# Optimization experiments

Hardware: AMD Instinct MI355X
Metric: run time of the kernel (lower is better)

The kernel has to match this reference:

```python
import jax, jax.numpy as jnp
import numpy as np

ANCHORS = np.array([[10,13],[16,30],[33,23],[30,61],[62,45],[59,119],[116,90],[156,198],[373,326]], dtype=np.float32)
ANCHOR_MASK = [[6,7,8],[3,4,5],[0,1,2]]
N_CLASSES = 80
IGNORE_THRESH = 0.5
MAX_TRUE = 128  # padded per-image GT box budget (replaces dynamic boolean indexing)


def _bce(logits, targets):
    # BCEWithLogits, elementwise: softplus(x) - x*z
    return jax.nn.softplus(logits) - logits * targets


def _decode(fm, anchors, input_shape):
    # fm: [B, A*(5+C), H, W] -> grid, raw [B,H,W,A,5+C], pred_xy, pred_wh
    B, _, H, W = fm.shape
    A = anchors.shape[0]
    raw = fm.reshape(B, A, 5 + N_CLASSES, H, W).transpose(0, 3, 4, 1, 2)
    gy, gx = jnp.meshgrid(jnp.arange(H, dtype=fm.dtype), jnp.arange(W, dtype=fm.dtype), indexing='ij')
    grid = jnp.stack([gx, gy], axis=-1)[None, :, :, None, :]  # [1,H,W,1,2] (x,y)
    gs = jnp.array([H, W], dtype=fm.dtype)
    pred_xy = (jax.nn.sigmoid(raw[..., :2]) + grid) / gs
    pred_wh = anchors[None, None, None, :, :] * jnp.exp(raw[..., 2:4]) / input_shape
    return grid, raw, pred_xy, pred_wh


def _gather_true(yt):
    # Pad/select up to MAX_TRUE GT boxes per image (object_mask == 1 cells).
    B = yt.shape[0]
    boxes = yt[..., :4].reshape(B, -1, 4)
    mask = yt[..., 4].reshape(B, -1)
    idx = jnp.argsort(-mask, axis=1)[:, :MAX_TRUE]            # positives first
    tb = jnp.take_along_axis(boxes, idx[..., None], axis=1)   # [B,K,4]
    valid = jnp.take_along_axis(mask, idx, axis=1) == 1.0     # [B,K]
    return tb, valid


def _best_iou(pred_box, tb, valid):
    # pred_box [B,H,W,A,4] (xywh), tb [B,K,4] -> best IoU over valid GT [B,H,W,A]
    p = pred_box[:, :, :, :, None, :]
    t = tb[:, None, None, None, :, :]
    p_min, p_max = p[..., :2] - p[..., 2:4] / 2, p[..., :2] + p[..., 2:4] / 2
    t_min, t_max = t[..., :2] - t[..., 2:4] / 2, t[..., :2] + t[..., 2:4] / 2
    inter = jnp.clip(jnp.minimum(p_max, t_max) - jnp.maximum(p_min, t_min), 0.0)
    inter_a = inter[..., 0] * inter[..., 1]
    pa = p[..., 2] * p[..., 3]
    ta = t[..., 2] * t[..., 3]
    iou = inter_a / (pa + ta - inter_a)
    iou = jnp.where(valid[:, None, None, None, :], iou, 0.0)
    return jnp.max(iou, axis=-1)


def _scale_loss(fm, yt, s, input_shape):
    B = fm.shape[0]
    anchors = jnp.asarray(ANCHORS[ANCHOR_MASK[s]])
    grid, raw, pxy, pwh = _decode(fm, anchors, input_shape)
    pred_box = jnp.concatenate([pxy, pwh], axis=-1)
    obj = yt[..., 4:5]
    tcls = yt[..., 5:]
    H, W = fm.shape[2], fm.shape[3]
    gs = jnp.array([H, W], dtype=fm.dtype)
    raw_txy = yt[..., :2] * gs - grid
    ratio = yt[..., 2:4] / anchors[None, None, None, :, :] * input_shape
    raw_twh = jnp.where(obj == 0, 0.0, jnp.log(jnp.where(obj == 0, 1.0, ratio)))
    box_scale = 2.0 - yt[..., 2:3] * yt[..., 3:4]
    tb, valid = _gather_true(yt)
    ignore = (_best_iou(pred_box, tb, valid) < IGNORE_THRESH).astype(fm.dtype)[..., None]
    xy_l = jnp.sum(obj * box_scale * _bce(raw[..., 0:2], raw_txy)) / B
    wh_l = jnp.sum(obj * box_scale * (raw[..., 2:4] - raw_twh) ** 2) / B
    bc = _bce(raw[..., 4:5], obj)
    conf_l = jnp.sum(obj * bc + (1.0 - obj) * bc * ignore) / B
    cls_l = jnp.sum(obj * _bce(raw[..., 5:], tcls)) / B
    return xy_l, wh_l, conf_l, cls_l


def _make_y_true(k, B, S):
    k1, k2, k3, k4 = jax.random.split(k, 4)
    xy = jax.random.uniform(k1, (B, S, S, 3, 2), minval=0.02, maxval=0.98)
    wh = jax.random.uniform(k2, (B, S, S, 3, 2), minval=0.02, maxval=0.4)
    obj = (jax.random.uniform(k3, (B, S, S, 3, 1)) < 0.005).astype(jnp.float32)
    cls = jax.nn.one_hot(jax.random.randint(k4, (B, S, S, 3), 0, N_CLASSES), N_CLASSES)
    return jnp.concatenate([xy, wh, obj, cls * obj], axis=-1)


def setup_inputs() -> dict:
    key = jax.random.key(0)
    ks = jax.random.split(key, 6)
    B = 16
    return {
        'yolo_out_0': jax.random.normal(ks[0], (B, 255, 19, 19), jnp.float32),
        'yolo_out_1': jax.random.normal(ks[1], (B, 255, 38, 38), jnp.float32),
        'yolo_out_2': jax.random.normal(ks[2], (B, 255, 76, 76), jnp.float32),
        'y_true_0': _make_y_true(ks[3], B, 19),
        'y_true_1': _make_y_true(ks[4], B, 38),
        'y_true_2': _make_y_true(ks[5], B, 76),
    }


def reference(yolo_out_0, yolo_out_1, yolo_out_2, y_true_0, y_true_1, y_true_2):
    outs = [yolo_out_0, yolo_out_1, yolo_out_2]
    yts = [y_true_0, y_true_1, y_true_2]
    input_shape = jnp.array([outs[0].shape[2] * 32, outs[0].shape[3] * 32], dtype=outs[0].dtype)
    lxy = lwh = lconf = lcls = 0.0
    for s in range(3):
        a, b, c, d = _scale_loss(outs[s], yts[s], s, input_shape)
        lxy, lwh, lconf, lcls = lxy + a, lwh + b, lconf + c, lcls + d
    total = lxy + lwh + lconf + lcls
    # [total, xy, wh, conf, class] (each was unsqueeze(0)'d in torch)
    return jnp.stack([total, lxy, lwh, lconf, lcls])
```

## Files before the change

### kernel.cpp

```cpp
#include <hip/hip_runtime.h>

#define MAX_TRUE 128

__device__ const float d_anch[3][3][2] = {
    {{116.f, 90.f}, {156.f, 198.f}, {373.f, 326.f}},
    {{30.f, 61.f}, {62.f, 45.f}, {59.f, 119.f}},
    {{10.f, 13.f}, {16.f, 30.f}, {33.f, 23.f}},
};

__device__ __forceinline__ float softplusf_(float x) {
    return fmaxf(x, 0.0f) + log1pf(expf(-fabsf(x)));
}
__device__ __forceinline__ float bcef_(float l, float t) {
    return softplusf_(l) - l * t;
}
__device__ __forceinline__ float sigmoidf_(float x) {
    return 1.0f / (1.0f + expf(-x));
}

__global__ void cand_kernel(const float* __restrict__ yt0, const float* __restrict__ yt1,
                            const float* __restrict__ yt2,
                            unsigned char* __restrict__ objmask,
                            float* __restrict__ chunkdata, int* __restrict__ chunkcnt) {
    __shared__ int wcnt[4];
    int bid = blockIdx.x, tid = threadIdx.x;
    int wid = tid >> 6, lane = tid & 63;
    int b, chunk, spb, objofs;
    const float* yt;
    if (bid < 80)       { b = bid / 5;  chunk = bid - b * 5;  spb = 1083;  objofs = 0;     yt = yt0; }
    else if (bid < 352) { int l = bid - 80;  b = l / 17; chunk = l - b * 17; spb = 4332;  objofs = 17328; yt = yt1; }
    else                { int l = bid - 352; b = l / 68; chunk = l - b * 68; spb = 17328; objofs = 86640; yt = yt2; }
    int cell = chunk * 256 + tid;
    bool valid = cell < spb;
    const float* src = yt + ((size_t)b * spb + cell) * 85;
    float obj = valid ? src[4] : 0.f;
    bool isobj = obj > 0.5f;
    if (valid) objmask[objofs + b * spb + cell] = isobj ? 1 : 0;
    unsigned long long m = __ballot(isobj);
    int wofs = __popcll(m & ((1ull << lane) - 1ull));
    if (lane == 0) wcnt[wid] = __popcll(m);
    __syncthreads();
    int base = 0;
    #pragma unroll
    for (int i = 0; i < 4; ++i) if (i < wid) base += wcnt[i];
    if (isobj) {
        int pos = base + wofs;
        float* d = chunkdata + ((size_t)bid * 256 + pos) * 5;
        d[0] = src[0];
        d[1] = src[1];
        d[2] = src[2];
        d[3] = src[3];
        ((int*)d)[4] = cell;
    }
    if (tid == 0) chunkcnt[bid] = wcnt[0] + wcnt[1] + wcnt[2] + wcnt[3];
}

__global__ void fused_kernel(const float* __restrict__ fm0, const float* __restrict__ fm1,
                             const float* __restrict__ fm2,
                             const float* __restrict__ yt0, const float* __restrict__ yt1,
                             const float* __restrict__ yt2,
                             const unsigned char* __restrict__ objmask,
                             const float* __restrict__ chunkdata, const int* __restrict__ chunkcnt,
                             float* __restrict__ partials, float* __restrict__ objpart) {
    __shared__ float4 sA[MAX_TRUE];
    __shared__ float sT[MAX_TRUE];
    __shared__ float wred[4][4];
    __shared__ int cnts[68];
    __shared__ int pre[69];
    int bid = blockIdx.x, tid = threadIdx.x;
    int wid = tid >> 6, lane = tid & 63;

    if (bid < 1488) {
        int s, local, lnb, Sdim, objofs, spb;
        const float* fm;
        if (bid < 96)       { s = 0; local = bid;       lnb = 2;  Sdim = 19; objofs = 0;     spb = 1083;  fm = fm0; }
        else if (bid < 384) { s = 1; local = bid - 96;  lnb = 6;  Sdim = 38; objofs = 17328; spb = 4332;  fm = fm1; }
        else                { s = 2; local = bid - 384; lnb = 23; Sdim = 76; objofs = 86640; spb = 17328; fm = fm2; }
        int ba = local / lnb;
        int chunk = local - ba * lnb;
        int a = ba % 3, b = ba / 3;
        int cbase, nch;
        if (s == 0)      { cbase = b * 5;        nch = 5;  }
        else if (s == 1) { cbase = 80 + b * 17;  nch = 17; }
        else             { cbase = 352 + b * 68; nch = 68; }
        if (tid < nch) cnts[tid] = chunkcnt[cbase + tid];
        __syncthreads();
        if (tid == 0) {
            int acc = 0;
            for (int c = 0; c < nch; ++c) { pre[c] = acc; acc += cnts[c]; }
            pre[nch] = acc;
        }
        __syncthreads();
        int total = pre[nch];
        int t128 = min(total, MAX_TRUE);
        if (tid < nch) {
            int n = cnts[tid], p0 = pre[tid];
            for (int j = 0; j < n; ++j) {
                int p = p0 + j;
                if (p >= MAX_TRUE) break;
                const float* e = chunkdata + ((size_t)(cbase + tid) * 256 + j) * 5;
                float x = e[0], y = e[1], w = e[2], h = e[3];
                float4 r;
                r.x = x - 0.5f * w; r.y = y - 0.5f * h;
                r.z = x + 0.5f * w; r.w = y + 0.5f * h;
                sA[p] = r;
                sT[p] = w * h;
            }
        }
        for (int p = t128 + tid; p < MAX_TRUE; p += 256) {
            sA[p] = make_float4(0.f, 0.f, 0.f, 0.f);
            sT[p] = 0.f;
        }
        __syncthreads();
        int kr = (t128 + 3) & ~3;
        int HW = Sdim * Sdim;
        int hw = chunk * 256 + tid;
        float lconf = 0.f;
        if (hw < HW) {
            int ob = objmask[objofs + b * spb + hw * 3 + a];
            const float* f = fm + ((size_t)(b * 255 + a * 85)) * HW + hw;
            float l0 = f[0], l1 = f[(size_t)HW], l2 = f[2 * (size_t)HW],
                  l3 = f[3 * (size_t)HW], l4 = f[4 * (size_t)HW];
            if (!ob) {
                int h = hw / Sdim, w = hw - h * Sdim;
                float aw = d_anch[s][a][0], ah = d_anch[s][a][1];
                const float inv_in = 1.0f / 608.0f;
                float px = (sigmoidf_(l0) + (float)w) / (float)Sdim;
                float py = (sigmoidf_(l1) + (float)h) / (float)Sdim;
                float pw = aw * expf(l2) * inv_in;
                float ph = ah * expf(l3) * inv_in;
                float pminx = px - 0.5f * pw, pmaxx = px + 0.5f * pw;
                float pminy = py - 0.5f * ph, pmaxy = py + 0.5f * ph;
                float pa = pw * ph;
                float m0 = 0.f, m1 = 0.f, m2 = 0.f, m3 = 0.f;
                for (int i = 0; i < kr; i += 4) {
                    float4 b0 = sA[i], b1 = sA[i + 1], b2 = sA[i + 2], b3 = sA[i + 3];
                    float t0 = sT[i], t1 = sT[i + 1], t2 = sT[i + 2], t3 = sT[i + 3];
                    float ix, iy;
                    ix = fmaxf(fminf(pmaxx, b0.z) - fmaxf(pminx, b0.x), 0.f);
                    iy = fmaxf(fminf(pmaxy, b0.w) - fmaxf(pminy, b0.y), 0.f);
                    m0 = fmaxf(m0, fmaf(3.0f, ix * iy, -t0));
                    ix = fmaxf(fminf(pmaxx, b1.z) - fmaxf(pminx, b1.x), 0.f);
                    iy = fmaxf(fminf(pmaxy, b1.w) - fmaxf(pminy, b1.y), 0.f);
                    m1 = fmaxf(m1, fmaf(3.0f, ix * iy, -t1));
                    ix = fmaxf(fminf(pmaxx, b2.z) - fmaxf(pminx, b2.x), 0.f);
                    iy = fmaxf(fminf(pmaxy, b2.w) - fmaxf(pminy, b2.y), 0.f);
                    m2 = fmaxf(m2, fmaf(3.0f, ix * iy, -t2));
                    ix = fmaxf(fminf(pmaxx, b3.z) - fmaxf(pminx, b3.x), 0.f);
                    iy = fmaxf(fminf(pmaxy, b3.w) - fmaxf(pminy, b3.y), 0.f);
                    m3 = fmaxf(m3, fmaf(3.0f, ix * iy, -t3));
                }
                float m = fmaxf(fmaxf(m0, m1), fmaxf(m2, m3));
                lconf = (m < pa) ? softplusf_(l4) : 0.f;
            }
        }
        #pragma unroll
        for (int o = 32; o > 0; o >>= 1)
            lconf += __shfl_down(lconf, o);
        if (lane == 0) wred[wid][0] = lconf;
        __syncthreads();
        if (tid == 0)
            partials[bid] = wred[0][0] + wred[1][0] + wred[2][0] + wred[3][0];
    } else {
        int cid = bid - 1488;
        int n = chunkcnt[cid];
        float* op = objpart + (size_t)cid * 4;
        if (n == 0) {
            if (tid == 0) { op[0] = 0.f; op[1] = 0.f; op[2] = 0.f; op[3] = 0.f; }
            return;
        }
        int s, b, spb, Sdim;
        const float *fm, *yt;
        if (cid < 80)       { s = 0; b = cid / 5;  spb = 1083;  Sdim = 19; fm = fm0; yt = yt0; }
        else if (cid < 352) { int l = cid - 80;  s = 1; b = l / 17; spb = 4332;  Sdim = 38; fm = fm1; yt = yt1; }
        else                { int l = cid - 352; s = 2; b = l / 68; spb = 17328; Sdim = 76; fm = fm2; yt = yt2; }
        int HW = Sdim * Sdim;
        float axy = 0.f, awh = 0.f, aconf = 0.f, acls = 0.f;
        for (int ci = wid; ci < n; ci += 4) {
            const float* cd = chunkdata + ((size_t)cid * 256 + ci) * 5;
            float x = cd[0], y = cd[1], w = cd[2], h = cd[3];
            int cell = ((const int*)cd)[4];
            int hw = cell / 3, a = cell - hw * 3;
            int hh = hw / Sdim, ww = hw - hh * Sdim;
            const float* f = fm + ((size_t)(b * 255 + a * 85)) * HW + hw;
            const float* yrow = yt + ((size_t)b * spb + cell) * 85;
            float cl = bcef_(f[(size_t)(5 + lane) * HW], yrow[5 + lane]);
            if (lane < 16) {
                int k2 = 64 + lane;
                cl += bcef_(f[(size_t)(5 + k2) * HW], yrow[5 + k2]);
            }
            acls += cl;
            float bscale = 2.f - w * h;
            if (lane < 5) {
                float lv = f[(size_t)lane * HW];
                if (lane == 0) axy += bscale * bcef_(lv, x * (float)Sdim - (float)ww);
                else if (lane == 1) axy += bscale * bcef_(lv, y * (float)Sdim - (float)hh);
                else if (lane == 2) {
                    float tw = logf(w / d_anch[s][a][0] * 608.f);
                    float d = lv - tw;
                    awh += bscale * d * d;
                } else if (lane == 3) {
                    float th = logf(h / d_anch[s][a][1] * 608.f);
                    float d = lv - th;
                    awh += bscale * d * d;
                } else {
                    aconf += bcef_(lv, 1.0f);
                }
            }
        }
        #pragma unroll
        for (int o = 32; o > 0; o >>= 1) {
            axy += __shfl_down(axy, o);
            awh += __shfl_down(awh, o);
            aconf += __shfl_down(aconf, o);
            acls += __shfl_down(acls, o);
        }
        if (lane == 0) {
            wred[wid][0] = axy; wred[wid][1] = awh;
            wred[wid][2] = aconf; wred[wid][3] = acls;
        }
        __syncthreads();
        if (tid == 0) {
            op[0] = wred[0][0] + wred[1][0] + wred[2][0] + wred[3][0];
            op[1] = wred[0][1] + wred[1][1] + wred[2][1] + wred[3][1];
            op[2] = wred[0][2] + wred[1][2] + wred[2][2] + wred[3][2];
            op[3] = wred[0][3] + wred[1][3] + wred[2][3] + wred[3][3];
        }
    }
}

__global__ void finalize_kernel(const float* __restrict__ partials,
                                const float* __restrict__ objpart,
                                float* __restrict__ out) {
    __shared__ float red[4][5];
    int tid = threadIdx.x;
    int wid = tid >> 6, lane = tid & 63;
    float cno = 0.f;
    for (int i = tid; i < 1488; i += 256) cno += partials[i];
    float xy = 0.f, wh = 0.f, co = 0.f, cl = 0.f;
    for (int i = tid; i < 1440; i += 256) {
        const float* op = objpart + (size_t)i * 4;
        xy += op[0]; wh += op[1]; co += op[2]; cl += op[3];
    }
    #pragma unroll
    for (int o = 32; o > 0; o >>= 1) {
        cno += __shfl_down(cno, o);
        xy += __shfl_down(xy, o);
        wh += __shfl_down(wh, o);
        co += __shfl_down(co, o);
        cl += __shfl_down(cl, o);
    }
    if (lane == 0) {
        red[wid][0] = cno; red[wid][1] = xy; red[wid][2] = wh;
        red[wid][3] = co;  red[wid][4] = cl;
    }
    __syncthreads();
    if (tid == 0) {
        float conf = 0.f, txy = 0.f, twh = 0.f, tcl = 0.f;
        for (int i = 0; i < 4; ++i) {
            conf += red[i][0] + red[i][3];
            txy += red[i][1]; twh += red[i][2]; tcl += red[i][4];
        }
        const float invB = 1.0f / 16.0f;
        float a0 = txy * invB;
        float a1 = twh * invB;
        float a2 = conf * invB;
        float a3 = tcl * invB;
        out[1] = a0; out[2] = a1; out[3] = a2; out[4] = a3;
        out[0] = a0 + a1 + a2 + a3;
    }
}

extern "C" void kernel_launch(void* const* d_in, const int* in_sizes, int n_in,
                              void* d_out, int out_size, void* d_ws, size_t ws_size,
                              hipStream_t stream) {
    const float* fm0 = (const float*)d_in[0];
    const float* fm1 = (const float*)d_in[1];
    const float* fm2 = (const float*)d_in[2];
    const float* yt0 = (const float*)d_in[3];
    const float* yt1 = (const float*)d_in[4];
    const float* yt2 = (const float*)d_in[5];
    float* out = (float*)d_out;

    char* ws = (char*)d_ws;
    int* chunkcnt = (int*)ws;
    float* partials = (float*)(ws + 5760);
    float* objpart = (float*)(ws + 11712);
    unsigned char* objmask = (unsigned char*)(ws + 34752);
    float* chunkdata = (float*)(ws + 398656);

    cand_kernel<<<1440, 256, 0, stream>>>(yt0, yt1, yt2, objmask, chunkdata, chunkcnt);
    fused_kernel<<<2928, 256, 0, stream>>>(fm0, fm1, fm2, yt0, yt1, yt2,
                                           objmask, chunkdata, chunkcnt, partials, objpart);
    finalize_kernel<<<1, 256, 0, stream>>>(partials, objpart, out);
}
```

Baseline: 41.32 us.

## Fuse object-cell loss computation into candidate compaction kernel

Moves the per-positive-cell xy/wh/conf/class loss work out of the second kernel and into the candidate-compaction kernel, reading the compacted boxes from shared memory instead of re-reading them from global memory. The second kernel now handles only the no-object confidence/IoU blocks, so its grid shrinks from 2928 to 1488 blocks. This shortens the second launch at the cost of a heavier first kernel that now also reads feature maps and uses extra shared memory.

```diff
diff --git a/kernel.cpp b/kernel.cpp
--- a/kernel.cpp
+++ b/kernel.cpp
@@ -18,18 +18,25 @@
     return 1.0f / (1.0f + expf(-x));
 }
 
-__global__ void cand_kernel(const float* __restrict__ yt0, const float* __restrict__ yt1,
-                            const float* __restrict__ yt2,
-                            unsigned char* __restrict__ objmask,
-                            float* __restrict__ chunkdata, int* __restrict__ chunkcnt) {
+__global__ void cand_obj_kernel(const float* __restrict__ yt0, const float* __restrict__ yt1,
+                                const float* __restrict__ yt2,
+                                const float* __restrict__ fm0, const float* __restrict__ fm1,
+                                const float* __restrict__ fm2,
+                                unsigned char* __restrict__ objmask,
+                                float* __restrict__ chunkdata, int* __restrict__ chunkcnt,
+                                float* __restrict__ objpart) {
     __shared__ int wcnt[4];
+    __shared__ float sc[256][5];
+    __shared__ float wred[4][4];
     int bid = blockIdx.x, tid = threadIdx.x;
     int wid = tid >> 6, lane = tid & 63;
-    int b, chunk, spb, objofs;
-    const float* yt;
-    if (bid < 80)       { b = bid / 5;  chunk = bid - b * 5;  spb = 1083;  objofs = 0;     yt = yt0; }
-    else if (bid < 352) { int l = bid - 80;  b = l / 17; chunk = l - b * 17; spb = 4332;  objofs = 17328; yt = yt1; }
-    else                { int l = bid - 352; b = l / 68; chunk = l - b * 68; spb = 17328; objofs = 86640; yt = yt2; }
+    int s, b, chunk, spb, objofs;
+    const float *yt, *fm;
+    if (bid < 80)       { s = 0; b = bid / 5;  chunk = bid - b * 5;  spb = 1083;  objofs = 0;     yt = yt0; fm = fm0; }
+    else if (bid < 352) { int l = bid - 80;  s = 1; b = l / 17; chunk = l - b * 17; spb = 4332;  objofs = 17328; yt = yt1; fm = fm1; }
+    else                { int l = bid - 352; s = 2; b = l / 68; chunk = l - b * 68; spb = 17328; objofs = 86640; yt = yt2; fm = fm2; }
+    int Sdim = (s == 0) ? 19 : ((s == 1) ? 38 : 76);
+    int HW = Sdim * Sdim;
     int cell = chunk * 256 + tid;
     bool valid = cell < spb;
     const float* src = yt + ((size_t)b * spb + cell) * 85;
@@ -43,190 +50,174 @@
     int base = 0;
     #pragma unroll
     for (int i = 0; i < 4; ++i) if (i < wid) base += wcnt[i];
+    int total = wcnt[0] + wcnt[1] + wcnt[2] + wcnt[3];
     if (isobj) {
         int pos = base + wofs;
+        float x = src[0], y = src[1], w = src[2], h = src[3];
         float* d = chunkdata + ((size_t)bid * 256 + pos) * 5;
-        d[0] = src[0];
-        d[1] = src[1];
-        d[2] = src[2];
-        d[3] = src[3];
+        d[0] = x; d[1] = y; d[2] = w; d[3] = h;
         ((int*)d)[4] = cell;
-    }
-    if (tid == 0) chunkcnt[bid] = wcnt[0] + wcnt[1] + wcnt[2] + wcnt[3];
-}
-
-__global__ void fused_kernel(const float* __restrict__ fm0, const float* __restrict__ fm1,
-                             const float* __restrict__ fm2,
-                             const float* __restrict__ yt0, const float* __restrict__ yt1,
-                             const float* __restrict__ yt2,
-                             const unsigned char* __restrict__ objmask,
-                             const float* __restrict__ chunkdata, const int* __restrict__ chunkcnt,
-                             float* __restrict__ partials, float* __restrict__ objpart) {
+        sc[pos][0] = x; sc[pos][1] = y; sc[pos][2] = w; sc[pos][3] = h;
+        ((int*)sc[pos])[4] = cell;
+    }
+    if (tid == 0) chunkcnt[bid] = total;
+    __syncthreads();
+
+    float axy = 0.f, awh = 0.f, aconf = 0.f, acls = 0.f;
+    for (int ci = wid; ci < total; ci += 4) {
+        float x = sc[ci][0], y = sc[ci][1], w = sc[ci][2], h = sc[ci][3];
+        int ccell = ((int*)sc[ci])[4];
+        int hw = ccell / 3, a = ccell - hw * 3;
+        int hh = hw / Sdim, ww = hw - hh * Sdim;
+        const float* f = fm + ((size_t)(b * 255 + a * 85)) * HW + hw;
+        const float* yrow = yt + ((size_t)b * spb + ccell) * 85;
+        float cl = bcef_(f[(size_t)(5 + lane) * HW], yrow[5 + lane]);
+        if (lane < 16) {
+            int k2 = 64 + lane;
+            cl += bcef_(f[(size_t)(5 + k2) * HW], yrow[5 + k2]);
+        }
+        acls += cl;
+        float bscale = 2.f - w * h;
+        if (lane < 5) {
+            float lv = f[(size_t)lane * HW];
+            if (lane == 0) axy += bscale * bcef_(lv, x * (float)Sdim - (float)ww);
+            else if (lane == 1) axy += bscale * bcef_(lv, y * (float)Sdim - (float)hh);
+            else if (lane == 2) {
+                float tw = logf(w / d_anch[s][a][0] * 608.f);
+                float d = lv - tw;
+                awh += bscale * d * d;
+            } else if (lane == 3) {
+                float th = logf(h / d_anch[s][a][1] * 608.f);
+                float d = lv - th;
+                awh += bscale * d * d;
+            } else {
+                aconf += bcef_(lv, 1.0f);
+            }
+        }
+    }
+    #pragma unroll
+    for (int o = 32; o > 0; o >>= 1) {
+        axy += __shfl_down(axy, o);
+        awh += __shfl_down(awh, o);
+        aconf += __shfl_down(aconf, o);
+        acls += __shfl_down(acls, o);
+    }
+    if (lane == 0) {
+        wred[wid][0] = axy; wred[wid][1] = awh;
+        wred[wid][2] = aconf; wred[wid][3] = acls;
+    }
+    __syncthreads();
+    if (tid == 0) {
+        float* op = objpart + (size_t)bid * 4;
+        op[0] = wred[0][0] + wred[1][0] + wred[2][0] + wred[3][0];
+        op[1] = wred[0][1] + wred[1][1] + wred[2][1] + wred[3][1];
+        op[2] = wred[0][2] + wred[1][2] + wred[2][2] + wred[3][2];
+        op[3] = wred[0][3] + wred[1][3] + wred[2][3] + wred[3][3];
+    }
+}
+
+__global__ void conf_kernel(const float* __restrict__ fm0, const float* __restrict__ fm1,
+                            const float* __restrict__ fm2,
+                            const unsigned char* __restrict__ objmask,
+                            const float* __restrict__ chunkdata, const int* __restrict__ chunkcnt,
+                            float* __restrict__ partials) {
     __shared__ float4 sA[MAX_TRUE];
     __shared__ float sT[MAX_TRUE];
-    __shared__ float wred[4][4];
+    __shared__ float wred[4];
     __shared__ int cnts[68];
     __shared__ int pre[69];
     int bid = blockIdx.x, tid = threadIdx.x;
     int wid = tid >> 6, lane = tid & 63;
-
-    if (bid < 1488) {
-        int s, local, lnb, Sdim, objofs, spb;
-        const float* fm;
-        if (bid < 96)       { s = 0; local = bid;       lnb = 2;  Sdim = 19; objofs = 0;     spb = 1083;  fm = fm0; }
-        else if (bid < 384) { s = 1; local = bid - 96;  lnb = 6;  Sdim = 38; objofs = 17328; spb = 4332;  fm = fm1; }
-        else                { s = 2; local = bid - 384; lnb = 23; Sdim = 76; objofs = 86640; spb = 17328; fm = fm2; }
-        int ba = local / lnb;
-        int chunk = local - ba * lnb;
-        int a = ba % 3, b = ba / 3;
-        int cbase, nch;
-        if (s == 0)      { cbase = b * 5;        nch = 5;  }
-        else if (s == 1) { cbase = 80 + b * 17;  nch = 17; }
-        else             { cbase = 352 + b * 68; nch = 68; }
-        if (tid < nch) cnts[tid] = chunkcnt[cbase + tid];
-        __syncthreads();
-        if (tid == 0) {
-            int acc = 0;
-            for (int c = 0; c < nch; ++c) { pre[c] = acc; acc += cnts[c]; }
-            pre[nch] = acc;
-        }
-        __syncthreads();
-        int total = pre[nch];
-        int t128 = min(total, MAX_TRUE);
-        if (tid < nch) {
-            int n = cnts[tid], p0 = pre[tid];
-            for (int j = 0; j < n; ++j) {
-                int p = p0 + j;
-                if (p >= MAX_TRUE) break;
-                const float* e = chunkdata + ((size_t)(cbase + tid) * 256 + j) * 5;
-                float x = e[0], y = e[1], w = e[2], h = e[3];
-                float4 r;
-                r.x = x - 0.5f * w; r.y = y - 0.5f * h;
-                r.z = x + 0.5f * w; r.w = y + 0.5f * h;
-                sA[p] = r;
-                sT[p] = w * h;
+    int s, local, lnb, Sdim, objofs, spb;
+    const float* fm;
+    if (bid < 96)       { s = 0; local = bid;       lnb = 2;  Sdim = 19; objofs = 0;     spb = 1083;  fm = fm0; }
+    else if (bid < 384) { s = 1; local = bid - 96;  lnb = 6;  Sdim = 38; objofs = 17328; spb = 4332;  fm = fm1; }
+    else                { s = 2; local = bid - 384; lnb = 23; Sdim = 76; objofs = 86640; spb = 17328; fm = fm2; }
+    int ba = local / lnb;
+    int chunk = local - ba * lnb;
+    int a = ba % 3, b = ba / 3;
+    int cbase, nch;
+    if (s == 0)      { cbase = b * 5;        nch = 5;  }
+    else if (s == 1) { cbase = 80 + b * 17;  nch = 17; }
+    else             { cbase = 352 + b * 68; nch = 68; }
+    if (tid < nch) cnts[tid] = chunkcnt[cbase + tid];
+    __syncthreads();
+    if (tid == 0) {
+        int acc = 0;
+        for (int c = 0; c < nch; ++c) { pre[c] = acc; acc += cnts[c]; }
+        pre[nch] = acc;
+    }
+    __syncthreads();
+    int total = pre[nch];
+    int t128 = min(total, MAX_TRUE);
+    if (tid < nch) {
+        int n = cnts[tid], p0 = pre[tid];
+        for (int j = 0; j < n; ++j) {
+            int p = p0 + j;
+            if (p >= MAX_TRUE) break;
+            const float* e = chunkdata + ((size_t)(cbase + tid) * 256 + j) * 5;
+            float x = e[0], y = e[1], w = e[2], h = e[3];
+            float4 r;
+            r.x = x - 0.5f * w; r.y = y - 0.5f * h;
+            r.z = x + 0.5f * w; r.w = y + 0.5f * h;
+            sA[p] = r;
+            sT[p] = w * h;
+        }
+    }
+    for (int p = t128 + tid; p < MAX_TRUE; p += 256) {
+        sA[p] = make_float4(0.f, 0.f, 0.f, 0.f);
+        sT[p] = 0.f;
+    }
+    __syncthreads();
+    int kr = (t128 + 3) & ~3;
+    int HW = Sdim * Sdim;
+    int hw = chunk * 256 + tid;
+    float lconf = 0.f;
+    if (hw < HW) {
+        int ob = objmask[objofs + b * spb + hw * 3 + a];
+        const float* f = fm + ((size_t)(b * 255 + a * 85)) * HW + hw;
+        float l0 = f[0], l1 = f[(size_t)HW], l2 = f[2 * (size_t)HW],
+              l3 = f[3 * (size_t)HW], l4 = f[4 * (size_t)HW];
+        if (!ob) {
+            int h = hw / Sdim, w = hw - h * Sdim;
+            float aw = d_anch[s][a][0], ah = d_anch[s][a][1];
+            const float inv_in = 1.0f / 608.0f;
+            float px = (sigmoidf_(l0) + (float)w) / (float)Sdim;
+            float py = (sigmoidf_(l1) + (float)h) / (float)Sdim;
+            float pw = aw * expf(l2) * inv_in;
+            float ph = ah * expf(l3) * inv_in;
+            float pminx = px - 0.5f * pw, pmaxx = px + 0.5f * pw;
+            float pminy = py - 0.5f * ph, pmaxy = py + 0.5f * ph;
+            float pa = pw * ph;
+            float m0 = 0.f, m1 = 0.f, m2 = 0.f, m3 = 0.f;
+            for (int i = 0; i < kr; i += 4) {
+                float4 b0 = sA[i], b1 = sA[i + 1], b2 = sA[i + 2], b3 = sA[i + 3];
+                float t0 = sT[i], t1 = sT[i + 1], t2 = sT[i + 2], t3 = sT[i + 3];
+                float ix, iy;
+                ix = fmaxf(fminf(pmaxx, b0.z) - fmaxf(pminx, b0.x), 0.f);
+                iy = fmaxf(fminf(pmaxy, b0.w) - fmaxf(pminy, b0.y), 0.f);
+                m0 = fmaxf(m0, fmaf(3.0f, ix * iy, -t0));
+                ix = fmaxf(fminf(pmaxx, b1.z) - fmaxf(pminx, b1.x), 0.f);
+                iy = fmaxf(fminf(pmaxy, b1.w) - fmaxf(pminy, b1.y), 0.f);
+                m1 = fmaxf(m1, fmaf(3.0f, ix * iy, -t1));
+                ix = fmaxf(fminf(pmaxx, b2.z) - fmaxf(pminx, b2.x), 0.f);
+                iy = fmaxf(fminf(pmaxy, b2.w) - fmaxf(pminy, b2.y), 0.f);
+                m2 = fmaxf(m2, fmaf(3.0f, ix * iy, -t2));
+                ix = fmaxf(fminf(pmaxx, b3.z) - fmaxf(pminx, b3.x), 0.f);
+                iy = fmaxf(fminf(pmaxy, b3.w) - fmaxf(pminy, b3.y), 0.f);
+                m3 = fmaxf(m3, fmaf(3.0f, ix * iy, -t3));
             }
-        }
-        for (int p = t128 + tid; p < MAX_TRUE; p += 256) {
-            sA[p] = make_float4(0.f, 0.f, 0.f, 0.f);
-            sT[p] = 0.f;
-        }
-        __syncthreads();
-        int kr = (t128 + 3) & ~3;
-        int HW = Sdim * Sdim;
-        int hw = chunk * 256 + tid;
-        float lconf = 0.f;
-        if (hw < HW) {
-            int ob = objmask[objofs + b * spb + hw * 3 + a];
-            const float* f = fm + ((size_t)(b * 255 + a * 85)) * HW + hw;
-            float l0 = f[0], l1 = f[(size_t)HW], l2 = f[2 * (size_t)HW],
-                  l3 = f[3 * (size_t)HW], l4 = f[4 * (size_t)HW];
-            if (!ob) {
-                int h = hw / Sdim, w = hw - h * Sdim;
-                float aw = d_anch[s][a][0], ah = d_anch[s][a][1];
-                const float inv_in = 1.0f / 608.0f;
-                float px = (sigmoidf_(l0) + (float)w) / (float)Sdim;
-                float py = (sigmoidf_(l1) + (float)h) / (float)Sdim;
-                float pw = aw * expf(l2) * inv_in;
-                float ph = ah * expf(l3) * inv_in;
-                float pminx = px - 0.5f * pw, pmaxx = px + 0.5f * pw;
-                float pminy = py - 0.5f * ph, pmaxy = py + 0.5f * ph;
-                float pa = pw * ph;
-                float m0 = 0.f, m1 = 0.f, m2 = 0.f, m3 = 0.f;
-                for (int i = 0; i < kr; i += 4) {
-                    float4 b0 = sA[i], b1 = sA[i + 1], b2 = sA[i + 2], b3 = sA[i + 3];
-                    float t0 = sT[i], t1 = sT[i + 1], t2 = sT[i + 2], t3 = sT[i + 3];
-                    float ix, iy;
-                    ix = fmaxf(fminf(pmaxx, b0.z) - fmaxf(pminx, b0.x), 0.f);
-                    iy = fmaxf(fminf(pmaxy, b0.w) - fmaxf(pminy, b0.y), 0.f);
-                    m0 = fmaxf(m0, fmaf(3.0f, ix * iy, -t0));
-                    ix = fmaxf(fminf(pmaxx, b1.z) - fmaxf(pminx, b1.x), 0.f);
-                    iy = fmaxf(fminf(pmaxy, b1.w) - fmaxf(pminy, b1.y), 0.f);
-                    m1 = fmaxf(m1, fmaf(3.0f, ix * iy, -t1));
-                    ix = fmaxf(fminf(pmaxx, b2.z) - fmaxf(pminx, b2.x), 0.f);
-                    iy = fmaxf(fminf(pmaxy, b2.w) - fmaxf(pminy, b2.y), 0.f);
-                    m2 = fmaxf(m2, fmaf(3.0f, ix * iy, -t2));
-                    ix = fmaxf(fminf(pmaxx, b3.z) - fmaxf(pminx, b3.x), 0.f);
-                    iy = fmaxf(fminf(pmaxy, b3.w) - fmaxf(pminy, b3.y), 0.f);
-                    m3 = fmaxf(m3, fmaf(3.0f, ix * iy, -t3));
-                }
-                float m = fmaxf(fmaxf(m0, m1), fmaxf(m2, m3));
-                lconf = (m < pa) ? softplusf_(l4) : 0.f;
-            }
-        }
-        #pragma unroll
-        for (int o = 32; o > 0; o >>= 1)
-            lconf += __shfl_down(lconf, o);
-        if (lane == 0) wred[wid][0] = lconf;
-        __syncthreads();
-        if (tid == 0)
-            partials[bid] = wred[0][0] + wred[1][0] + wred[2][0] + wred[3][0];
-    } else {
-        int cid = bid - 1488;
-        int n = chunkcnt[cid];
-        float* op = objpart + (size_t)cid * 4;
-        if (n == 0) {
-            if (tid == 0) { op[0] = 0.f; op[1] = 0.f; op[2] = 0.f; op[3] = 0.f; }
-            return;
-        }
-        int s, b, spb, Sdim;
-        const float *fm, *yt;
-        if (cid < 80)       { s = 0; b = cid / 5;  spb = 1083;  Sdim = 19; fm = fm0; yt = yt0; }
-        else if (cid < 352) { int l = cid - 80;  s = 1; b = l / 17; spb = 4332;  Sdim = 38; fm = fm1; yt = yt1; }
-        else                { int l = cid - 352; s = 2; b = l / 68; spb = 17328; Sdim = 76; fm = fm2; yt = yt2; }
-        int HW = Sdim * Sdim;
-        float axy = 0.f, awh = 0.f, aconf = 0.f, acls = 0.f;
-        for (int ci = wid; ci < n; ci += 4) {
-            const float* cd = chunkdata + ((size_t)cid * 256 + ci) * 5;
-            float x = cd[0], y = cd[1], w = cd[2], h = cd[3];
-            int cell = ((const int*)cd)[4];
-            int hw = cell / 3, a = cell - hw * 3;
-            int hh = hw / Sdim, ww = hw - hh * Sdim;
-            const float* f = fm + ((size_t)(b * 255 + a * 85)) * HW + hw;
-            const float* yrow = yt + ((size_t)b * spb + cell) * 85;
-            float cl = bcef_(f[(size_t)(5 + lane) * HW], yrow[5 + lane]);
-            if (lane < 16) {
-                int k2 = 64 + lane;
-                cl += bcef_(f[(size_t)(5 + k2) * HW], yrow[5 + k2]);
-            }
-            acls += cl;
-            float bscale = 2.f - w * h;
-            if (lane < 5) {
-                float lv = f[(size_t)lane * HW];
-                if (lane == 0) axy += bscale * bcef_(lv, x * (float)Sdim - (float)ww);
-                else if (lane == 1) axy += bscale * bcef_(lv, y * (float)Sdim - (float)hh);
-                else if (lane == 2) {
-                    float tw = logf(w / d_anch[s][a][0] * 608.f);
-                    float d = lv - tw;
-                    awh += bscale * d * d;
-                } else if (lane == 3) {
-                    float th = logf(h / d_anch[s][a][1] * 608.f);
-                    float d = lv - th;
-                    awh += bscale * d * d;
-                } else {
-                    aconf += bcef_(lv, 1.0f);
-                }
-            }
-        }
-        #pragma unroll
-        for (int o = 32; o > 0; o >>= 1) {
-            axy += __shfl_down(axy, o);
-            awh += __shfl_down(awh, o);
-            aconf += __shfl_down(aconf, o);
-            acls += __shfl_down(acls, o);
-        }
-        if (lane == 0) {
-            wred[wid][0] = axy; wred[wid][1] = awh;
-            wred[wid][2] = aconf; wred[wid][3] = acls;
-        }
-        __syncthreads();
-        if (tid == 0) {
-            op[0] = wred[0][0] + wred[1][0] + wred[2][0] + wred[3][0];
-            op[1] = wred[0][1] + wred[1][1] + wred[2][1] + wred[3][1];
-            op[2] = wred[0][2] + wred[1][2] + wred[2][2] + wred[3][2];
-            op[3] = wred[0][3] + wred[1][3] + wred[2][3] + wred[3][3];
-        }
-    }
+            float m = fmaxf(fmaxf(m0, m1), fmaxf(m2, m3));
+            lconf = (m < pa) ? softplusf_(l4) : 0.f;
+        }
+    }
+    #pragma unroll
+    for (int o = 32; o > 0; o >>= 1)
+        lconf += __shfl_down(lconf, o);
+    if (lane == 0) wred[wid] = lconf;
+    __syncthreads();
+    if (tid == 0)
+        partials[bid] = wred[0] + wred[1] + wred[2] + wred[3];
 }
 
 __global__ void finalize_kernel(const float* __restrict__ partials,
@@ -289,8 +280,9 @@
     unsigned char* objmask = (unsigned char*)(ws + 34752);
     float* chunkdata = (float*)(ws + 398656);
 
-    cand_kernel<<<1440, 256, 0, stream>>>(yt0, yt1, yt2, objmask, chunkdata, chunkcnt);
-    fused_kernel<<<2928, 256, 0, stream>>>(fm0, fm1, fm2, yt0, yt1, yt2,
-                                           objmask, chunkdata, chunkcnt, partials, objpart);
+    cand_obj_kernel<<<1440, 256, 0, stream>>>(yt0, yt1, yt2, fm0, fm1, fm2,
+                                              objmask, chunkdata, chunkcnt, objpart);
+    conf_kernel<<<1488, 256, 0, stream>>>(fm0, fm1, fm2, objmask,
+                                          chunkdata, chunkcnt, partials);
     finalize_kernel<<<1, 256, 0, stream>>>(partials, objpart, out);
 }
```

Result: slower. 45.62 us (+10.4%).

## Replace global object mask with shared bitmask and process two cells per thread

Applied to the files above, without the earlier changes.

Removes the global per-cell object mask written by the candidate kernel. Each no-object block now rebuilds a shared-memory bitmask from the compacted candidate list using atomicOr. Each block covers 512 cells (two per thread), which roughly halves the number of no-object blocks and the repeated per-block GT box staging. The serial prefix sum becomes a parallel scan, and only the confidence logit is loaded for object cells. The tradeoff is more work per thread, fewer blocks in flight, and an extra pass over the candidates in every block.

```diff
diff --git a/kernel.cpp b/kernel.cpp
--- a/kernel.cpp
+++ b/kernel.cpp
@@ -20,22 +20,20 @@
 
 __global__ void cand_kernel(const float* __restrict__ yt0, const float* __restrict__ yt1,
                             const float* __restrict__ yt2,
-                            unsigned char* __restrict__ objmask,
                             float* __restrict__ chunkdata, int* __restrict__ chunkcnt) {
     __shared__ int wcnt[4];
     int bid = blockIdx.x, tid = threadIdx.x;
     int wid = tid >> 6, lane = tid & 63;
-    int b, chunk, spb, objofs;
+    int b, chunk, spb;
     const float* yt;
-    if (bid < 80)       { b = bid / 5;  chunk = bid - b * 5;  spb = 1083;  objofs = 0;     yt = yt0; }
-    else if (bid < 352) { int l = bid - 80;  b = l / 17; chunk = l - b * 17; spb = 4332;  objofs = 17328; yt = yt1; }
-    else                { int l = bid - 352; b = l / 68; chunk = l - b * 68; spb = 17328; objofs = 86640; yt = yt2; }
+    if (bid < 80)       { b = bid / 5;  chunk = bid - b * 5;  spb = 1083;  yt = yt0; }
+    else if (bid < 352) { int l = bid - 80;  b = l / 17; chunk = l - b * 17; spb = 4332;  yt = yt1; }
+    else                { int l = bid - 352; b = l / 68; chunk = l - b * 68; spb = 17328; yt = yt2; }
     int cell = chunk * 256 + tid;
     bool valid = cell < spb;
     const float* src = yt + ((size_t)b * spb + cell) * 85;
     float obj = valid ? src[4] : 0.f;
     bool isobj = obj > 0.5f;
-    if (valid) objmask[objofs + b * spb + cell] = isobj ? 1 : 0;
     unsigned long long m = __ballot(isobj);
     int wofs = __popcll(m & ((1ull << lane) - 1ull));
     if (lane == 0) wcnt[wid] = __popcll(m);
@@ -59,23 +57,23 @@
                              const float* __restrict__ fm2,
                              const float* __restrict__ yt0, const float* __restrict__ yt1,
                              const float* __restrict__ yt2,
-                             const unsigned char* __restrict__ objmask,
                              const float* __restrict__ chunkdata, const int* __restrict__ chunkcnt,
                              float* __restrict__ partials, float* __restrict__ objpart) {
     __shared__ float4 sA[MAX_TRUE];
     __shared__ float sT[MAX_TRUE];
     __shared__ float wred[4][4];
     __shared__ int cnts[68];
-    __shared__ int pre[69];
+    __shared__ int pre[68];
+    __shared__ unsigned int obit[16];
     int bid = blockIdx.x, tid = threadIdx.x;
     int wid = tid >> 6, lane = tid & 63;
 
-    if (bid < 1488) {
-        int s, local, lnb, Sdim, objofs, spb;
+    if (bid < 768) {
+        int s, local, lnb, Sdim;
         const float* fm;
-        if (bid < 96)       { s = 0; local = bid;       lnb = 2;  Sdim = 19; objofs = 0;     spb = 1083;  fm = fm0; }
-        else if (bid < 384) { s = 1; local = bid - 96;  lnb = 6;  Sdim = 38; objofs = 17328; spb = 4332;  fm = fm1; }
-        else                { s = 2; local = bid - 384; lnb = 23; Sdim = 76; objofs = 86640; spb = 17328; fm = fm2; }
+        if (bid < 48)       { s = 0; local = bid;       lnb = 1;  Sdim = 19; fm = fm0; }
+        else if (bid < 192) { s = 1; local = bid - 48;  lnb = 3;  Sdim = 38; fm = fm1; }
+        else                { s = 2; local = bid - 192; lnb = 12; Sdim = 76; fm = fm2; }
         int ba = local / lnb;
         int chunk = local - ba * lnb;
         int a = ba % 3, b = ba / 3;
@@ -84,27 +82,40 @@
         else if (s == 1) { cbase = 80 + b * 17;  nch = 17; }
         else             { cbase = 352 + b * 68; nch = 68; }
         if (tid < nch) cnts[tid] = chunkcnt[cbase + tid];
-        __syncthreads();
-        if (tid == 0) {
-            int acc = 0;
-            for (int c = 0; c < nch; ++c) { pre[c] = acc; acc += cnts[c]; }
-            pre[nch] = acc;
-        }
-        __syncthreads();
-        int total = pre[nch];
+        if (tid < 16) obit[tid] = 0u;
+        __syncthreads();
+        if (tid < nch) pre[tid] = cnts[tid];
+        __syncthreads();
+        for (int off = 1; off < nch; off <<= 1) {
+            int v = 0;
+            if (tid < nch) { v = pre[tid]; if (tid >= off) v += pre[tid - off]; }
+            __syncthreads();
+            if (tid < nch) pre[tid] = v;
+            __syncthreads();
+        }
+        int total = pre[nch - 1];
         int t128 = min(total, MAX_TRUE);
         if (tid < nch) {
-            int n = cnts[tid], p0 = pre[tid];
+            int n = cnts[tid];
+            int p0 = pre[tid] - n;
+            const float* cptr = chunkdata + (size_t)(cbase + tid) * 256 * 5;
             for (int j = 0; j < n; ++j) {
+                const float* e = cptr + j * 5;
+                int c = ((const int*)e)[4];
+                if (c % 3 == a) {
+                    int rel = c / 3 - chunk * 512;
+                    if (rel >= 0 && rel < 512)
+                        atomicOr(&obit[rel >> 5], 1u << (rel & 31));
+                }
                 int p = p0 + j;
-                if (p >= MAX_TRUE) break;
-                const float* e = chunkdata + ((size_t)(cbase + tid) * 256 + j) * 5;
-                float x = e[0], y = e[1], w = e[2], h = e[3];
-                float4 r;
-                r.x = x - 0.5f * w; r.y = y - 0.5f * h;
-                r.z = x + 0.5f * w; r.w = y + 0.5f * h;
-                sA[p] = r;
-                sT[p] = w * h;
+                if (p < MAX_TRUE) {
+                    float x = e[0], y = e[1], w = e[2], h = e[3];
+                    float4 r;
+                    r.x = x - 0.5f * w; r.y = y - 0.5f * h;
+                    r.z = x + 0.5f * w; r.w = y + 0.5f * h;
+                    sA[p] = r;
+                    sT[p] = w * h;
+                }
             }
         }
         for (int p = t128 + tid; p < MAX_TRUE; p += 256) {
@@ -114,44 +125,49 @@
         __syncthreads();
         int kr = (t128 + 3) & ~3;
         int HW = Sdim * Sdim;
-        int hw = chunk * 256 + tid;
+        float aw = d_anch[s][a][0], ah = d_anch[s][a][1];
         float lconf = 0.f;
-        if (hw < HW) {
-            int ob = objmask[objofs + b * spb + hw * 3 + a];
-            const float* f = fm + ((size_t)(b * 255 + a * 85)) * HW + hw;
-            float l0 = f[0], l1 = f[(size_t)HW], l2 = f[2 * (size_t)HW],
-                  l3 = f[3 * (size_t)HW], l4 = f[4 * (size_t)HW];
-            if (!ob) {
-                int h = hw / Sdim, w = hw - h * Sdim;
-                float aw = d_anch[s][a][0], ah = d_anch[s][a][1];
-                const float inv_in = 1.0f / 608.0f;
-                float px = (sigmoidf_(l0) + (float)w) / (float)Sdim;
-                float py = (sigmoidf_(l1) + (float)h) / (float)Sdim;
-                float pw = aw * expf(l2) * inv_in;
-                float ph = ah * expf(l3) * inv_in;
-                float pminx = px - 0.5f * pw, pmaxx = px + 0.5f * pw;
-                float pminy = py - 0.5f * ph, pmaxy = py + 0.5f * ph;
-                float pa = pw * ph;
-                float m0 = 0.f, m1 = 0.f, m2 = 0.f, m3 = 0.f;
-                for (int i = 0; i < kr; i += 4) {
-                    float4 b0 = sA[i], b1 = sA[i + 1], b2 = sA[i + 2], b3 = sA[i + 3];
-                    float t0 = sT[i], t1 = sT[i + 1], t2 = sT[i + 2], t3 = sT[i + 3];
-                    float ix, iy;
-                    ix = fmaxf(fminf(pmaxx, b0.z) - fmaxf(pminx, b0.x), 0.f);
-                    iy = fmaxf(fminf(pmaxy, b0.w) - fmaxf(pminy, b0.y), 0.f);
-                    m0 = fmaxf(m0, fmaf(3.0f, ix * iy, -t0));
-                    ix = fmaxf(fminf(pmaxx, b1.z) - fmaxf(pminx, b1.x), 0.f);
-                    iy = fmaxf(fminf(pmaxy, b1.w) - fmaxf(pminy, b1.y), 0.f);
-                    m1 = fmaxf(m1, fmaf(3.0f, ix * iy, -t1));
-                    ix = fmaxf(fminf(pmaxx, b2.z) - fmaxf(pminx, b2.x), 0.f);
-                    iy = fmaxf(fminf(pmaxy, b2.w) - fmaxf(pminy, b2.y), 0.f);
-                    m2 = fmaxf(m2, fmaf(3.0f, ix * iy, -t2));
-                    ix = fmaxf(fminf(pmaxx, b3.z) - fmaxf(pminx, b3.x), 0.f);
-                    iy = fmaxf(fminf(pmaxy, b3.w) - fmaxf(pminy, b3.y), 0.f);
-                    m3 = fmaxf(m3, fmaf(3.0f, ix * iy, -t3));
+        #pragma unroll
+        for (int half = 0; half < 2; ++half) {
+            int rel = half * 256 + tid;
+            int hw = chunk * 512 + rel;
+            if (hw < HW) {
+                int ob = (obit[rel >> 5] >> (rel & 31)) & 1;
+                const float* f = fm + ((size_t)(b * 255 + a * 85)) * HW + hw;
+                float l4 = f[4 * (size_t)HW];
+                if (!ob) {
+                    float l0 = f[0], l1 = f[(size_t)HW], l2 = f[2 * (size_t)HW],
+                          l3 = f[3 * (size_t)HW];
+                    int h = hw / Sdim, w = hw - h * Sdim;
+                    const float inv_in = 1.0f / 608.0f;
+                    float px = (sigmoidf_(l0) + (float)w) / (float)Sdim;
+                    float py = (sigmoidf_(l1) + (float)h) / (float)Sdim;
+                    float pw = aw * expf(l2) * inv_in;
+                    float ph = ah * expf(l3) * inv_in;
+                    float pminx = px - 0.5f * pw, pmaxx = px + 0.5f * pw;
+                    float pminy = py - 0.5f * ph, pmaxy = py + 0.5f * ph;
+                    float pa = pw * ph;
+                    float m0 = 0.f, m1 = 0.f, m2 = 0.f, m3 = 0.f;
+                    for (int i = 0; i < kr; i += 4) {
+                        float4 b0 = sA[i], b1 = sA[i + 1], b2 = sA[i + 2], b3 = sA[i + 3];
+                        float t0 = sT[i], t1 = sT[i + 1], t2 = sT[i + 2], t3 = sT[i + 3];
+                        float ix, iy;
+                        ix = fmaxf(fminf(pmaxx, b0.z) - fmaxf(pminx, b0.x), 0.f);
+                        iy = fmaxf(fminf(pmaxy, b0.w) - fmaxf(pminy, b0.y), 0.f);
+                        m0 = fmaxf(m0, fmaf(3.0f, ix * iy, -t0));
+                        ix = fmaxf(fminf(pmaxx, b1.z) - fmaxf(pminx, b1.x), 0.f);
+                        iy = fmaxf(fminf(pmaxy, b1.w) - fmaxf(pminy, b1.y), 0.f);
+                        m1 = fmaxf(m1, fmaf(3.0f, ix * iy, -t1));
+                        ix = fmaxf(fminf(pmaxx, b2.z) - fmaxf(pminx, b2.x), 0.f);
+                        iy = fmaxf(fminf(pmaxy, b2.w) - fmaxf(pminy, b2.y), 0.f);
+                        m2 = fmaxf(m2, fmaf(3.0f, ix * iy, -t2));
+                        ix = fmaxf(fminf(pmaxx, b3.z) - fmaxf(pminx, b3.x), 0.f);
+                        iy = fmaxf(fminf(pmaxy, b3.w) - fmaxf(pminy, b3.y), 0.f);
+                        m3 = fmaxf(m3, fmaf(3.0f, ix * iy, -t3));
+                    }
+                    float m = fmaxf(fmaxf(m0, m1), fmaxf(m2, m3));
+                    lconf += (m < pa) ? softplusf_(l4) : 0.f;
                 }
-                float m = fmaxf(fmaxf(m0, m1), fmaxf(m2, m3));
-                lconf = (m < pa) ? softplusf_(l4) : 0.f;
             }
         }
         #pragma unroll
@@ -162,7 +178,7 @@
         if (tid == 0)
             partials[bid] = wred[0][0] + wred[1][0] + wred[2][0] + wred[3][0];
     } else {
-        int cid = bid - 1488;
+        int cid = bid - 768;
         int n = chunkcnt[cid];
         float* op = objpart + (size_t)cid * 4;
         if (n == 0) {
@@ -236,7 +252,7 @@
     int tid = threadIdx.x;
     int wid = tid >> 6, lane = tid & 63;
     float cno = 0.f;
-    for (int i = tid; i < 1488; i += 256) cno += partials[i];
+    for (int i = tid; i < 768; i += 256) cno += partials[i];
     float xy = 0.f, wh = 0.f, co = 0.f, cl = 0.f;
     for (int i = tid; i < 1440; i += 256) {
         const float* op = objpart + (size_t)i * 4;
@@ -285,12 +301,11 @@
     char* ws = (char*)d_ws;
     int* chunkcnt = (int*)ws;
     float* partials = (float*)(ws + 5760);
-    float* objpart = (float*)(ws + 11712);
-    unsigned char* objmask = (unsigned char*)(ws + 34752);
-    float* chunkdata = (float*)(ws + 398656);
-
-    cand_kernel<<<1440, 256, 0, stream>>>(yt0, yt1, yt2, objmask, chunkdata, chunkcnt);
-    fused_kernel<<<2928, 256, 0, stream>>>(fm0, fm1, fm2, yt0, yt1, yt2,
-                                           objmask, chunkdata, chunkcnt, partials, objpart);
+    float* objpart = (float*)(ws + 8832);
+    float* chunkdata = (float*)(ws + 31872);
+
+    cand_kernel<<<1440, 256, 0, stream>>>(yt0, yt1, yt2, chunkdata, chunkcnt);
+    fused_kernel<<<2208, 256, 0, stream>>>(fm0, fm1, fm2, yt0, yt1, yt2,
+                                           chunkdata, chunkcnt, partials, objpart);
     finalize_kernel<<<1, 256, 0, stream>>>(partials, objpart, out);
 }
```

After: 41.91 us. About the same (+1.4%).
